# Kernel tuning notes

Hardware: AMD Instinct MI355X
Metric: run time of the kernel (lower is better)

## Reference

```python
import jax, jax.numpy as jnp
import numpy as np

WS = 7   # w_size
K = 9    # k_neighbors


def setup_inputs() -> dict:
    key = jax.random.key(0)
    ks = jax.random.split(key, 6)
    B, C, H, W = 16, 64, 112, 112
    Cf = C // 4
    return {
        'x_in': jax.random.normal(ks[0], (B, C, H, W), jnp.float32),
        'Wf': jax.random.normal(ks[1], (Cf, C), jnp.float32) / np.sqrt(C).astype(np.float32),
        'bf': jnp.zeros((Cf,), jnp.float32),
        'Wp': jax.random.normal(ks[2], (C, Cf), jnp.float32) / np.sqrt(Cf).astype(np.float32),
        'bp': jnp.zeros((C,), jnp.float32),
        'W1': jax.random.normal(ks[3], (4, 2), jnp.float32) / np.sqrt(2.0).astype(np.float32),
        'b1': jnp.zeros((4,), jnp.float32),
        'W2': jax.random.normal(ks[4], (1, 4), jnp.float32) / 2.0,
        'b2': jnp.zeros((1,), jnp.float32),
        'sigma': jnp.asarray(4.0, jnp.float32),
        'alpha': jnp.asarray(0.5, jnp.float32),
    }


def reference(x_in, Wf, bf, Wp, bp, W1, b1, W2, b2, sigma, alpha):
    B, C, H, W = x_in.shape
    w, h = H // WS, W // WS                      # per-window spatial dims
    Bp, N = B * WS * WS, w * h                   # num windows, nodes per window
    # window partition: b c (Wg w) (Hg h) -> (b Wg Hg) c w h
    x = x_in.reshape(B, C, WS, w, WS, h).transpose(0, 2, 4, 1, 3, 5).reshape(Bp, C, w, h)
    # 1x1 conv f: dim -> dim//4
    f = jnp.einsum('bchw,oc->bohw', x, Wf) + bf[None, :, None, None]
    Cf = f.shape[1]
    xf = f.reshape(Bp, Cf, N).transpose(0, 2, 1)          # [Bp, N, Cf] node features
    # all-pairs cosine similarity (torch eps=1e-8)
    xn = xf / jnp.maximum(jnp.linalg.norm(xf, axis=-1, keepdims=True), 1e-8)
    sim_feat = jnp.einsum('bnc,bmc->bnm', xn, xn)         # [Bp, N, N]
    # spatial gaussian similarity
    ii, jj = jnp.meshgrid(jnp.arange(w), jnp.arange(h), indexing='ij')
    coords = jnp.stack([ii, jj], -1).reshape(N, 2).astype(jnp.float32)
    dist = jnp.sqrt(jnp.sum((coords[:, None] - coords[None]) ** 2, -1))
    sim_dist = jnp.exp(-dist ** 2 / (2.0 * sigma ** 2))   # [N, N]
    combined = alpha * sim_feat + (1.0 - alpha) * sim_dist[None]
    _, idx = jax.lax.top_k(combined, K)                   # [Bp, N, K] neighbor ids
    # gather neighbor messages; edges of node n are exactly its K top-k columns
    msg = xf[jnp.arange(Bp)[:, None, None], idx]          # [Bp, N, K, Cf]
    sf = jnp.take_along_axis(sim_feat, idx, axis=-1)      # edge cosine sim
    sd = sim_dist[jnp.arange(N)[:, None], idx]            # edge spatial sim
    pair = jnp.stack([sf, sd], -1)                        # [Bp, N, K, 2]
    hdn = jax.nn.silu(pair @ W1.T + b1)
    wgt = jax.nn.sigmoid(hdn @ W2.T + b2)[..., 0]         # [Bp, N, K]
    # scatter_add over edge_index[0] == per-source sum over its K edges
    wn = wgt / (jnp.sum(wgt, -1, keepdims=True) + 1e-12)
    out = jnp.einsum('bnk,bnkc->bnc', wn, msg)            # [Bp, N, Cf]
    out = out.reshape(Bp, w, h, Cf).transpose(0, 3, 1, 2)
    # window un-partition: (b Wg Hg) c w h -> b c (Wg w) (Hg h)
    out = out.reshape(B, WS, WS, Cf, w, h).transpose(0, 3, 1, 4, 2, 5).reshape(B, Cf, H, W)
    # 1x1 conv p: dim//4 -> dim, then flatten(2)
    y = jnp.einsum('bchw,oc->bohw', out, Wp) + bp[None, :, None, None]
    return y.reshape(B, C, H * W)
```

## Files before the change

kernel.cpp:

```cpp
#include <hip/hip_runtime.h>
#include <math.h>

#define CC    64
#define CF    16
#define NPIX  256
#define KK    9
#define HWQ   12544
#define WWQ   112
#define NTILE 784
#define MBLK  128

__global__ __launch_bounds__(64, 4) void feat_k(
    const float* __restrict__ x_in, const float* __restrict__ Wf,
    const float* __restrict__ bf,
    float* __restrict__ xn_g, float* __restrict__ nrm_g)
{
    __shared__ float s_Wt[CC * CF];
    __shared__ float s_bf[CF];
    const int tid = threadIdx.x;
    for (int idx = tid; idx < CC * CF; idx += 64) {
        int c = idx >> 4, o = idx & 15;
        s_Wt[idx] = Wf[o * CC + c];
    }
    if (tid < CF) s_bf[tid] = bf[tid];
    __syncthreads();

    const int p    = blockIdx.x * 64 + tid;
    const int tile = p >> 8, pix = p & 255;
    const int bb = tile / 49, ssb = tile % 49;
    const int s1 = ssb / 7, s2 = ssb % 7;
    const int gy = s1 * 16 + (pix >> 4), gx = s2 * 16 + (pix & 15);
    const float* xb = x_in + (size_t)bb * CC * HWQ + (size_t)gy * WWQ + gx;

    float fv[CF];
    #pragma unroll
    for (int o = 0; o < CF; ++o) fv[o] = 0.0f;
    #pragma unroll 8
    for (int c = 0; c < CC; ++c) {
        float xv = xb[(size_t)c * HWQ];
        const float4* w4 = reinterpret_cast<const float4*>(&s_Wt[c << 4]);
        float4 w0 = w4[0], w1 = w4[1], w2 = w4[2], w3 = w4[3];
        fv[0]  = fmaf(xv, w0.x, fv[0]);  fv[1]  = fmaf(xv, w0.y, fv[1]);
        fv[2]  = fmaf(xv, w0.z, fv[2]);  fv[3]  = fmaf(xv, w0.w, fv[3]);
        fv[4]  = fmaf(xv, w1.x, fv[4]);  fv[5]  = fmaf(xv, w1.y, fv[5]);
        fv[6]  = fmaf(xv, w1.z, fv[6]);  fv[7]  = fmaf(xv, w1.w, fv[7]);
        fv[8]  = fmaf(xv, w2.x, fv[8]);  fv[9]  = fmaf(xv, w2.y, fv[9]);
        fv[10] = fmaf(xv, w2.z, fv[10]); fv[11] = fmaf(xv, w2.w, fv[11]);
        fv[12] = fmaf(xv, w3.x, fv[12]); fv[13] = fmaf(xv, w3.y, fv[13]);
        fv[14] = fmaf(xv, w3.z, fv[14]); fv[15] = fmaf(xv, w3.w, fv[15]);
    }
    #pragma unroll
    for (int o = 0; o < CF; ++o) fv[o] += s_bf[o];

    float ss2 = 0.0f;
    #pragma unroll
    for (int o = 0; o < CF; ++o) ss2 = fmaf(fv[o], fv[o], ss2);
    float nrm = fmaxf(sqrtf(ss2), 1e-8f);

    float xn[CF];
    #pragma unroll
    for (int o = 0; o < CF; ++o) xn[o] = fv[o] / nrm;

    float4* dst = reinterpret_cast<float4*>(xn_g + (size_t)p * CF);
    dst[0] = make_float4(xn[0],  xn[1],  xn[2],  xn[3]);
    dst[1] = make_float4(xn[4],  xn[5],  xn[6],  xn[7]);
    dst[2] = make_float4(xn[8],  xn[9],  xn[10], xn[11]);
    dst[3] = make_float4(xn[12], xn[13], xn[14], xn[15]);
    nrm_g[p] = nrm;
}

#define DOT16(dot, a0, a1, a2, a3)                                   \
    dot = fmaf(xnr[0],  (a0).x, dot); dot = fmaf(xnr[1],  (a0).y, dot); \
    dot = fmaf(xnr[2],  (a0).z, dot); dot = fmaf(xnr[3],  (a0).w, dot); \
    dot = fmaf(xnr[4],  (a1).x, dot); dot = fmaf(xnr[5],  (a1).y, dot); \
    dot = fmaf(xnr[6],  (a1).z, dot); dot = fmaf(xnr[7],  (a1).w, dot); \
    dot = fmaf(xnr[8],  (a2).x, dot); dot = fmaf(xnr[9],  (a2).y, dot); \
    dot = fmaf(xnr[10], (a2).z, dot); dot = fmaf(xnr[11], (a2).w, dot); \
    dot = fmaf(xnr[12], (a3).x, dot); dot = fmaf(xnr[13], (a3).y, dot); \
    dot = fmaf(xnr[14], (a3).z, dot); dot = fmaf(xnr[15], (a3).w, dot);

#define TOP9_INSERT(cv, ci) {                                        \
    const bool g0 = (cv) > tv0; const bool g1 = (cv) > tv1;          \
    const bool g2 = (cv) > tv2; const bool g3 = (cv) > tv3;          \
    const bool g4 = (cv) > tv4; const bool g5 = (cv) > tv5;          \
    const bool g6 = (cv) > tv6; const bool g7 = (cv) > tv7;          \
    const bool g8 = (cv) > tv8;                                      \
    const float nv0 = g0 ? (cv) : tv0;                               \
    const float nv1 = __builtin_amdgcn_fmed3f((cv), tv0, tv1);       \
    const float nv2 = __builtin_amdgcn_fmed3f((cv), tv1, tv2);       \
    const float nv3 = __builtin_amdgcn_fmed3f((cv), tv2, tv3);       \
    const float nv4 = __builtin_amdgcn_fmed3f((cv), tv3, tv4);       \
    const float nv5 = __builtin_amdgcn_fmed3f((cv), tv4, tv5);       \
    const float nv6 = __builtin_amdgcn_fmed3f((cv), tv5, tv6);       \
    const float nv7 = __builtin_amdgcn_fmed3f((cv), tv6, tv7);       \
    const float nv8 = __builtin_amdgcn_fmed3f((cv), tv7, tv8);       \
    const int nt0 = g0 ? (ci) : ti0;                                 \
    const int nt1 = g0 ? ti0 : (g1 ? (ci) : ti1);                    \
    const int nt2 = g1 ? ti1 : (g2 ? (ci) : ti2);                    \
    const int nt3 = g2 ? ti2 : (g3 ? (ci) : ti3);                    \
    const int nt4 = g3 ? ti3 : (g4 ? (ci) : ti4);                    \
    const int nt5 = g4 ? ti4 : (g5 ? (ci) : ti5);                    \
    const int nt6 = g5 ? ti5 : (g6 ? (ci) : ti6);                    \
    const int nt7 = g6 ? ti6 : (g7 ? (ci) : ti7);                    \
    const int nt8 = g7 ? ti7 : (g8 ? (ci) : ti8);                    \
    tv0 = nv0; tv1 = nv1; tv2 = nv2; tv3 = nv3; tv4 = nv4;           \
    tv5 = nv5; tv6 = nv6; tv7 = nv7; tv8 = nv8;                      \
    ti0 = nt0; ti1 = nt1; ti2 = nt2; ti3 = nt3; ti4 = nt4;           \
    ti5 = nt5; ti6 = nt6; ti7 = nt7; ti8 = nt8; }

#define SIM_ITER(MJ) {                                               \
    const int m = mbase + (MJ);                                      \
    const float4* xm4 = reinterpret_cast<const float4*>(&s_xn[m][0]);\
    const float4 a0 = xm4[0], a1 = xm4[1], a2 = xm4[2], a3 = xm4[3]; \
    float dot = 0.0f;                                                \
    DOT16(dot, a0, a1, a2, a3);                                      \
    const int dj = pj - (MJ);                                        \
    const float sdA = s_tabA[d2i + dj * dj];                         \
    const float comb = __fadd_rn(__fmul_rn(alpha, dot), sdA);        \
    TOP9_INSERT(comb, m); }

__global__ __launch_bounds__(MBLK, 4) void gnn_main(
    const float* __restrict__ xn_g, const float* __restrict__ nrm_g,
    const float* __restrict__ Wp,   const float* __restrict__ bp,
    const float* __restrict__ W1,   const float* __restrict__ b1,
    const float* __restrict__ W2,   const float* __restrict__ b2,
    const float* __restrict__ sigma_p, const float* __restrict__ alpha_p,
    float* __restrict__ y)
{
    __shared__ float s_xn[NPIX][CF];
    __shared__ float s_nrm[NPIX];
    __shared__ float s_tab[451];
    __shared__ float s_tabA[451];

    const int bid  = blockIdx.x;
    const int tile = bid >> 1;
    const int hlf  = bid & 1;
    const int bb = tile / 49, ssb = tile % 49;
    const int s1 = ssb / 7, s2 = ssb % 7;
    const int tid = threadIdx.x;

    const float alpha = alpha_p[0];
    const float oma   = 1.0f - alpha;
    const float sig   = sigma_p[0];
    const float denom = 2.0f * sig * sig;

    for (int t = tid; t < 451; t += MBLK) {
        float dd = sqrtf((float)t);
        float v  = expf((-(dd * dd)) / denom);
        s_tab[t]  = v;
        s_tabA[t] = __fmul_rn(oma, v);
    }
    const float* xt = xn_g + (size_t)tile * NPIX * CF;
    {
        const float4* src = reinterpret_cast<const float4*>(xt);
        float4*       dst = reinterpret_cast<float4*>(&s_xn[0][0]);
        #pragma unroll
        for (int i = 0; i < 8; ++i) dst[tid + i * MBLK] = src[tid + i * MBLK];
        const float* nsrc = nrm_g + (size_t)tile * NPIX;
        s_nrm[tid]        = nsrc[tid];
        s_nrm[tid + MBLK] = nsrc[tid + MBLK];
    }
    float W1r[8], b1r[4], W2r[4];
    #pragma unroll
    for (int h = 0; h < 8; ++h) W1r[h] = W1[h];
    #pragma unroll
    for (int h = 0; h < 4; ++h) { b1r[h] = b1[h]; W2r[h] = W2[h]; }
    const float b2r = b2[0];
    __syncthreads();

    const int r  = hlf * MBLK + tid;
    const int pi = r >> 4, pj = r & 15;

    float xnr[CF];
    {
        const float4* xr4 = reinterpret_cast<const float4*>(&s_xn[r][0]);
        float4 r0 = xr4[0], r1 = xr4[1], r2 = xr4[2], r3 = xr4[3];
        xnr[0]=r0.x;  xnr[1]=r0.y;  xnr[2]=r0.z;  xnr[3]=r0.w;
        xnr[4]=r1.x;  xnr[5]=r1.y;  xnr[6]=r1.z;  xnr[7]=r1.w;
        xnr[8]=r2.x;  xnr[9]=r2.y;  xnr[10]=r2.z; xnr[11]=r2.w;
        xnr[12]=r3.x; xnr[13]=r3.y; xnr[14]=r3.z; xnr[15]=r3.w;
    }

    float tv0,tv1,tv2,tv3,tv4,tv5,tv6,tv7,tv8;
    int   ti0,ti1,ti2,ti3,ti4,ti5,ti6,ti7,ti8;
    tv0=tv1=tv2=tv3=tv4=tv5=tv6=tv7=tv8 = -INFINITY;
    ti0=ti1=ti2=ti3=ti4=ti5=ti6=ti7=ti8 = 0;

    #pragma unroll 1
    for (int mi = 0; mi < 16; ++mi) {
        const int di  = pi - mi;
        const int d2i = di * di;
        const int mbase = mi << 4;
        SIM_ITER(0)  SIM_ITER(1)  SIM_ITER(2)  SIM_ITER(3)
        SIM_ITER(4)  SIM_ITER(5)  SIM_ITER(6)  SIM_ITER(7)
        SIM_ITER(8)  SIM_ITER(9)  SIM_ITER(10) SIM_ITER(11)
        SIM_ITER(12) SIM_ITER(13) SIM_ITER(14) SIM_ITER(15)
    }

    const float tv[KK] = {tv0,tv1,tv2,tv3,tv4,tv5,tv6,tv7,tv8};
    const int   ti[KK] = {ti0,ti1,ti2,ti3,ti4,ti5,ti6,ti7,ti8};

    float wk[KK];
    float wsum = 0.0f;
    #pragma unroll
    for (int k = 0; k < KK; ++k) {
        int m = ti[k];
        int di = pi - (m >> 4);
        int dj = pj - (m & 15);
        float sd = s_tab[di * di + dj * dj];
        float sf = (tv[k] - __fmul_rn(oma, sd)) / alpha;
        float hsum = b2r;
        #pragma unroll
        for (int h = 0; h < 4; ++h) {
            float z  = fmaf(sf, W1r[2 * h], fmaf(sd, W1r[2 * h + 1], b1r[h]));
            float sg = 1.0f / (1.0f + expf(-z));
            hsum = fmaf(z * sg, W2r[h], hsum);
        }
        float wg = 1.0f / (1.0f + expf(-hsum));
        wk[k] = wg;
        wsum += wg;
    }
    wsum += 1e-12f;

    float outv[CF];
    #pragma unroll
    for (int o = 0; o < CF; ++o) outv[o] = 0.0f;
    #pragma unroll
    for (int k = 0; k < KK; ++k) {
        const int m = ti[k];
        const float wnm = (wk[k] / wsum) * s_nrm[m];
        const float4* xf4 = reinterpret_cast<const float4*>(&s_xn[m][0]);
        float4 m0 = xf4[0], m1 = xf4[1], m2 = xf4[2], m3 = xf4[3];
        outv[0]  = fmaf(wnm, m0.x, outv[0]);  outv[1]  = fmaf(wnm, m0.y, outv[1]);
        outv[2]  = fmaf(wnm, m0.z, outv[2]);  outv[3]  = fmaf(wnm, m0.w, outv[3]);
        outv[4]  = fmaf(wnm, m1.x, outv[4]);  outv[5]  = fmaf(wnm, m1.y, outv[5]);
        outv[6]  = fmaf(wnm, m1.z, outv[6]);  outv[7]  = fmaf(wnm, m1.w, outv[7]);
        outv[8]  = fmaf(wnm, m2.x, outv[8]);  outv[9]  = fmaf(wnm, m2.y, outv[9]);
        outv[10] = fmaf(wnm, m2.z, outv[10]); outv[11] = fmaf(wnm, m2.w, outv[11]);
        outv[12] = fmaf(wnm, m3.x, outv[12]); outv[13] = fmaf(wnm, m3.y, outv[13]);
        outv[14] = fmaf(wnm, m3.z, outv[14]); outv[15] = fmaf(wnm, m3.w, outv[15]);
    }

    const int gy = s1 * 16 + pi, gx = s2 * 16 + pj;
    float* yb = y + (size_t)bb * CC * HWQ + (size_t)gy * WWQ + gx;
    #pragma unroll 4
    for (int o = 0; o < CC; ++o) {
        const float4* w4 = reinterpret_cast<const float4*>(&Wp[o * CF]);
        float4 w0 = w4[0], w1 = w4[1], w2 = w4[2], w3 = w4[3];
        float acc = 0.0f;
        acc = fmaf(outv[0],  w0.x, acc); acc = fmaf(outv[1],  w0.y, acc);
        acc = fmaf(outv[2],  w0.z, acc); acc = fmaf(outv[3],  w0.w, acc);
        acc = fmaf(outv[4],  w1.x, acc); acc = fmaf(outv[5],  w1.y, acc);
        acc = fmaf(outv[6],  w1.z, acc); acc = fmaf(outv[7],  w1.w, acc);
        acc = fmaf(outv[8],  w2.x, acc); acc = fmaf(outv[9],  w2.y, acc);
        acc = fmaf(outv[10], w2.z, acc); acc = fmaf(outv[11], w2.w, acc);
        acc = fmaf(outv[12], w3.x, acc); acc = fmaf(outv[13], w3.y, acc);
        acc = fmaf(outv[14], w3.z, acc); acc = fmaf(outv[15], w3.w, acc);
        yb[(size_t)o * HWQ] = acc + bp[o];
    }
}

__global__ __launch_bounds__(256) void gnn_fused(
    const float* __restrict__ x_in, const float* __restrict__ Wf,
    const float* __restrict__ bf,   const float* __restrict__ Wp,
    const float* __restrict__ bp,   const float* __restrict__ W1,
    const float* __restrict__ b1,   const float* __restrict__ W2,
    const float* __restrict__ b2,   const float* __restrict__ sigma_p,
    const float* __restrict__ alpha_p, float* __restrict__ y)
{
    __shared__ float s_xf[NPIX][CF];
    __shared__ float s_xn[NPIX][CF];
    __shared__ float s_W[CC * CF];
    __shared__ float s_table[451];
    __shared__ float s_bias[CC];

    const int bpi = blockIdx.x;
    const int bb  = bpi / 49;
    const int ssb = bpi % 49;
    const int s1  = ssb / 7, s2 = ssb % 7;
    const int tid = threadIdx.x;
    const int pi  = tid >> 4, pj = tid & 15;
    const int gy  = s1 * 16 + pi, gx = s2 * 16 + pj;

    const float alpha = alpha_p[0];
    const float oma   = 1.0f - alpha;
    const float sig   = sigma_p[0];
    const float denom = 2.0f * sig * sig;

    for (int t = tid; t < CF * CC; t += NPIX) s_W[t] = Wf[t];
    if (tid < CF) s_bias[tid] = bf[tid];
    for (int t = tid; t < 451; t += NPIX) {
        float dd = sqrtf((float)t);
        s_table[t] = expf((-(dd * dd)) / denom);
    }
    float W1r[8], b1r[4], W2r[4];
    #pragma unroll
    for (int h = 0; h < 8; ++h) W1r[h] = W1[h];
    #pragma unroll
    for (int h = 0; h < 4; ++h) { b1r[h] = b1[h]; W2r[h] = W2[h]; }
    const float b2r = b2[0];
    __syncthreads();

    const float* xb = x_in + (size_t)bb * CC * HWQ + (size_t)gy * WWQ + gx;
    float fv[CF];
    #pragma unroll
    for (int o = 0; o < CF; ++o) fv[o] = 0.0f;
    for (int c = 0; c < CC; ++c) {
        float xv = xb[(size_t)c * HWQ];
        #pragma unroll
        for (int o = 0; o < CF; ++o)
            fv[o] = fmaf(xv, s_W[o * CC + c], fv[o]);
    }
    #pragma unroll
    for (int o = 0; o < CF; ++o) fv[o] += s_bias[o];

    float ss2 = 0.0f;
    #pragma unroll
    for (int o = 0; o < CF; ++o) ss2 = fmaf(fv[o], fv[o], ss2);
    float nrm = fmaxf(sqrtf(ss2), 1e-8f);

    float xnr[CF];
    #pragma unroll
    for (int o = 0; o < CF; ++o) {
        xnr[o] = fv[o] / nrm;
        s_xf[tid][o] = fv[o];
        s_xn[tid][o] = xnr[o];
    }
    __syncthreads();

    float tv[KK]; int ti[KK];
    #pragma unroll
    for (int k = 0; k < KK; ++k) { tv[k] = -INFINITY; ti[k] = 0; }

    for (int m = 0; m < NPIX; ++m) {
        const float4* xm4 = reinterpret_cast<const float4*>(&s_xn[m][0]);
        float4 a0 = xm4[0], a1 = xm4[1], a2 = xm4[2], a3 = xm4[3];
        float dot = 0.0f;
        dot = fmaf(xnr[0],  a0.x, dot); dot = fmaf(xnr[1],  a0.y, dot);
        dot = fmaf(xnr[2],  a0.z, dot); dot = fmaf(xnr[3],  a0.w, dot);
        dot = fmaf(xnr[4],  a1.x, dot); dot = fmaf(xnr[5],  a1.y, dot);
        dot = fmaf(xnr[6],  a1.z, dot); dot = fmaf(xnr[7],  a1.w, dot);
        dot = fmaf(xnr[8],  a2.x, dot); dot = fmaf(xnr[9],  a2.y, dot);
        dot = fmaf(xnr[10], a2.z, dot); dot = fmaf(xnr[11], a2.w, dot);
        dot = fmaf(xnr[12], a3.x, dot); dot = fmaf(xnr[13], a3.y, dot);
        dot = fmaf(xnr[14], a3.z, dot); dot = fmaf(xnr[15], a3.w, dot);

        int di = pi - (m >> 4);
        int dj = pj - (m & 15);
        float sd = s_table[di * di + dj * dj];
        float comb = __fadd_rn(__fmul_rn(alpha, dot), __fmul_rn(oma, sd));

        if (comb > tv[KK - 1]) {
            float cv = comb; int ci = m;
            #pragma unroll
            for (int t = KK - 1; t >= 0; --t) {
                bool g = (cv > tv[t]);
                float ov = tv[t]; int oi = ti[t];
                if (g) {
                    if (t + 1 < KK) { tv[t + 1] = ov; ti[t + 1] = oi; }
                    tv[t] = cv; ti[t] = ci;
                }
            }
        }
    }

    float wk[KK];
    float wsum = 0.0f;
    #pragma unroll
    for (int k = 0; k < KK; ++k) {
        int m = ti[k];
        int di = pi - (m >> 4);
        int dj = pj - (m & 15);
        float sd = s_table[di * di + dj * dj];
        float sf = (tv[k] - __fmul_rn(oma, sd)) / alpha;
        float hsum = b2r;
        #pragma unroll
        for (int h = 0; h < 4; ++h) {
            float z  = fmaf(sf, W1r[2 * h], fmaf(sd, W1r[2 * h + 1], b1r[h]));
            float sg = 1.0f / (1.0f + expf(-z));
            hsum = fmaf(z * sg, W2r[h], hsum);
        }
        float wg = 1.0f / (1.0f + expf(-hsum));
        wk[k] = wg;
        wsum += wg;
    }
    wsum += 1e-12f;

    float outv[CF];
    #pragma unroll
    for (int o = 0; o < CF; ++o) outv[o] = 0.0f;
    #pragma unroll
    for (int k = 0; k < KK; ++k) {
        float wn = wk[k] / wsum;
        int m = ti[k];
        const float4* xf4 = reinterpret_cast<const float4*>(&s_xf[m][0]);
        float4 m0 = xf4[0], m1 = xf4[1], m2 = xf4[2], m3 = xf4[3];
        outv[0]  = fmaf(wn, m0.x, outv[0]);  outv[1]  = fmaf(wn, m0.y, outv[1]);
        outv[2]  = fmaf(wn, m0.z, outv[2]);  outv[3]  = fmaf(wn, m0.w, outv[3]);
        outv[4]  = fmaf(wn, m1.x, outv[4]);  outv[5]  = fmaf(wn, m1.y, outv[5]);
        outv[6]  = fmaf(wn, m1.z, outv[6]);  outv[7]  = fmaf(wn, m1.w, outv[7]);
        outv[8]  = fmaf(wn, m2.x, outv[8]);  outv[9]  = fmaf(wn, m2.y, outv[9]);
        outv[10] = fmaf(wn, m2.z, outv[10]); outv[11] = fmaf(wn, m2.w, outv[11]);
        outv[12] = fmaf(wn, m3.x, outv[12]); outv[13] = fmaf(wn, m3.y, outv[13]);
        outv[14] = fmaf(wn, m3.z, outv[14]); outv[15] = fmaf(wn, m3.w, outv[15]);
    }

    __syncthreads();
    for (int t = tid; t < CC * CF; t += NPIX) s_W[t] = Wp[t];
    if (tid < CC) s_bias[tid] = bp[tid];
    __syncthreads();

    float* yb = y + (size_t)bb * CC * HWQ + (size_t)gy * WWQ + gx;
    for (int o = 0; o < CC; ++o) {
        float acc = 0.0f;
        #pragma unroll
        for (int c = 0; c < CF; ++c)
            acc = fmaf(outv[c], s_W[o * CF + c], acc);
        yb[(size_t)o * HWQ] = acc + s_bias[o];
    }
}

extern "C" void kernel_launch(void* const* d_in, const int* in_sizes, int n_in,
                              void* d_out, int out_size, void* d_ws, size_t ws_size,
                              hipStream_t stream) {
    const float* x_in  = (const float*)d_in[0];
    const float* Wf    = (const float*)d_in[1];
    const float* bf    = (const float*)d_in[2];
    const float* Wp    = (const float*)d_in[3];
    const float* bp    = (const float*)d_in[4];
    const float* W1    = (const float*)d_in[5];
    const float* b1    = (const float*)d_in[6];
    const float* W2    = (const float*)d_in[7];
    const float* b2    = (const float*)d_in[8];
    const float* sigma = (const float*)d_in[9];
    const float* alpha = (const float*)d_in[10];
    float* y = (float*)d_out;

    const size_t need = (size_t)(NTILE * NPIX * CF + NTILE * NPIX) * sizeof(float);
    if (ws_size >= need) {
        float* xn_g  = (float*)d_ws;
        float* nrm_g = xn_g + (size_t)NTILE * NPIX * CF;
        feat_k<<<3136, 64, 0, stream>>>(x_in, Wf, bf, xn_g, nrm_g);
        gnn_main<<<NTILE * 2, MBLK, 0, stream>>>(xn_g, nrm_g, Wp, bp, W1, b1,
                                                 W2, b2, sigma, alpha, y);
    } else {
        gnn_fused<<<NTILE, NPIX, 0, stream>>>(x_in, Wf, bf, Wp, bp, W1, b1, W2,
                                              b2, sigma, alpha, y);
    }
}
```

Before: 131.1 us.

## Split top-k candidate scan across two thread halves with global partial merge

Each block grows to 256 threads, and the two 128-thread halves scan disjoint halves of the 256 candidate nodes, so every row keeps its own partial top-9. The upper half writes its partial list to a new workspace buffer. After a block barrier the lower half reads it back and merges it with TOP9_INSERT before computing edge weights and the output projection. The aim is more parallelism and latency hiding in the serial similarity and top-k scan. In exchange it needs more workspace, adds global-memory traffic and a barrier, and tighter launch bounds that could cause register spills; the old path is kept as a fallback when workspace is small.

```diff
diff --git a/kernel.cpp b/kernel.cpp
--- a/kernel.cpp
+++ b/kernel.cpp
@@ -8,6 +8,7 @@
 #define HWQ   12544
 #define WWQ   112
 #define NTILE 784
+#define NROWS (NTILE * NPIX)
 #define MBLK  128
 
 __global__ __launch_bounds__(64, 4) void feat_k(
@@ -119,12 +120,19 @@
     const float comb = __fadd_rn(__fmul_rn(alpha, dot), sdA);        \
     TOP9_INSERT(comb, m); }
 
-__global__ __launch_bounds__(MBLK, 4) void gnn_main(
+#define SIM_ROW16()                                                  \
+        SIM_ITER(0)  SIM_ITER(1)  SIM_ITER(2)  SIM_ITER(3)           \
+        SIM_ITER(4)  SIM_ITER(5)  SIM_ITER(6)  SIM_ITER(7)           \
+        SIM_ITER(8)  SIM_ITER(9)  SIM_ITER(10) SIM_ITER(11)          \
+        SIM_ITER(12) SIM_ITER(13) SIM_ITER(14) SIM_ITER(15)
+
+__global__ __launch_bounds__(256, 7) void gnn_split(
     const float* __restrict__ xn_g, const float* __restrict__ nrm_g,
     const float* __restrict__ Wp,   const float* __restrict__ bp,
     const float* __restrict__ W1,   const float* __restrict__ b1,
     const float* __restrict__ W2,   const float* __restrict__ b2,
     const float* __restrict__ sigma_p, const float* __restrict__ alpha_p,
+    float* __restrict__ pval, int* __restrict__ pidx,
     float* __restrict__ y)
 {
     __shared__ float s_xn[NPIX][CF];
@@ -138,13 +146,15 @@
     const int bb = tile / 49, ssb = tile % 49;
     const int s1 = ssb / 7, s2 = ssb % 7;
     const int tid = threadIdx.x;
+    const int rl  = tid & 127;
+    const int ch  = tid >> 7;
 
     const float alpha = alpha_p[0];
     const float oma   = 1.0f - alpha;
     const float sig   = sigma_p[0];
     const float denom = 2.0f * sig * sig;
 
-    for (int t = tid; t < 451; t += MBLK) {
+    for (int t = tid; t < 451; t += 256) {
         float dd = sqrtf((float)t);
         float v  = expf((-(dd * dd)) / denom);
         s_tab[t]  = v;
@@ -155,10 +165,8 @@
         const float4* src = reinterpret_cast<const float4*>(xt);
         float4*       dst = reinterpret_cast<float4*>(&s_xn[0][0]);
         #pragma unroll
-        for (int i = 0; i < 8; ++i) dst[tid + i * MBLK] = src[tid + i * MBLK];
-        const float* nsrc = nrm_g + (size_t)tile * NPIX;
-        s_nrm[tid]        = nsrc[tid];
-        s_nrm[tid + MBLK] = nsrc[tid + MBLK];
+        for (int i = 0; i < 4; ++i) dst[tid + i * 256] = src[tid + i * 256];
+        s_nrm[tid] = nrm_g[(size_t)tile * NPIX + tid];
     }
     float W1r[8], b1r[4], W2r[4];
     #pragma unroll
@@ -168,8 +176,9 @@
     const float b2r = b2[0];
     __syncthreads();
 
-    const int r  = hlf * MBLK + tid;
+    const int r  = hlf * 128 + rl;
     const int pi = r >> 4, pj = r & 15;
+    const int gRow = tile * NPIX + r;
 
     float xnr[CF];
     {
@@ -186,15 +195,35 @@
     tv0=tv1=tv2=tv3=tv4=tv5=tv6=tv7=tv8 = -INFINITY;
     ti0=ti1=ti2=ti3=ti4=ti5=ti6=ti7=ti8 = 0;
 
+    const int mi0 = ch << 3;
     #pragma unroll 1
-    for (int mi = 0; mi < 16; ++mi) {
+    for (int q = 0; q < 8; ++q) {
+        const int mi  = mi0 + q;
         const int di  = pi - mi;
         const int d2i = di * di;
         const int mbase = mi << 4;
-        SIM_ITER(0)  SIM_ITER(1)  SIM_ITER(2)  SIM_ITER(3)
-        SIM_ITER(4)  SIM_ITER(5)  SIM_ITER(6)  SIM_ITER(7)
-        SIM_ITER(8)  SIM_ITER(9)  SIM_ITER(10) SIM_ITER(11)
-        SIM_ITER(12) SIM_ITER(13) SIM_ITER(14) SIM_ITER(15)
+        SIM_ROW16()
+    }
+
+    if (ch == 1) {
+        pval[0 * NROWS + gRow] = tv0; pidx[0 * NROWS + gRow] = ti0;
+        pval[1 * NROWS + gRow] = tv1; pidx[1 * NROWS + gRow] = ti1;
+        pval[2 * NROWS + gRow] = tv2; pidx[2 * NROWS + gRow] = ti2;
+        pval[3 * NROWS + gRow] = tv3; pidx[3 * NROWS + gRow] = ti3;
+        pval[4 * NROWS + gRow] = tv4; pidx[4 * NROWS + gRow] = ti4;
+        pval[5 * NROWS + gRow] = tv5; pidx[5 * NROWS + gRow] = ti5;
+        pval[6 * NROWS + gRow] = tv6; pidx[6 * NROWS + gRow] = ti6;
+        pval[7 * NROWS + gRow] = tv7; pidx[7 * NROWS + gRow] = ti7;
+        pval[8 * NROWS + gRow] = tv8; pidx[8 * NROWS + gRow] = ti8;
+    }
+    __syncthreads();
+    if (ch == 1) return;
+
+    #pragma unroll
+    for (int k = 0; k < KK; ++k) {
+        const float bv = pval[k * NROWS + gRow];
+        const int   bi = pidx[k * NROWS + gRow];
+        TOP9_INSERT(bv, bi);
     }
 
     const float tv[KK] = {tv0,tv1,tv2,tv3,tv4,tv5,tv6,tv7,tv8};
@@ -260,6 +289,144 @@
     }
 }
 
+__global__ __launch_bounds__(MBLK, 4) void gnn_main_r5(
+    const float* __restrict__ xn_g, const float* __restrict__ nrm_g,
+    const float* __restrict__ Wp,   const float* __restrict__ bp,
+    const float* __restrict__ W1,   const float* __restrict__ b1,
+    const float* __restrict__ W2,   const float* __restrict__ b2,
+    const float* __restrict__ sigma_p, const float* __restrict__ alpha_p,
+    float* __restrict__ y)
+{
+    __shared__ float s_xn[NPIX][CF];
+    __shared__ float s_nrm[NPIX];
+    __shared__ float s_tab[451];
+    __shared__ float s_tabA[451];
+
+    const int bid  = blockIdx.x;
+    const int tile = bid >> 1;
+    const int hlf  = bid & 1;
+    const int bb = tile / 49, ssb = tile % 49;
+    const int s1 = ssb / 7, s2 = ssb % 7;
+    const int tid = threadIdx.x;
+
+    const float alpha = alpha_p[0];
+    const float oma   = 1.0f - alpha;
+    const float sig   = sigma_p[0];
+    const float denom = 2.0f * sig * sig;
+
+    for (int t = tid; t < 451; t += MBLK) {
+        float dd = sqrtf((float)t);
+        float v  = expf((-(dd * dd)) / denom);
+        s_tab[t]  = v;
+        s_tabA[t] = __fmul_rn(oma, v);
+    }
+    const float* xt = xn_g + (size_t)tile * NPIX * CF;
+    {
+        const float4* src = reinterpret_cast<const float4*>(xt);
+        float4*       dst = reinterpret_cast<float4*>(&s_xn[0][0]);
+        #pragma unroll
+        for (int i = 0; i < 8; ++i) dst[tid + i * MBLK] = src[tid + i * MBLK];
+        const float* nsrc = nrm_g + (size_t)tile * NPIX;
+        s_nrm[tid]        = nsrc[tid];
+        s_nrm[tid + MBLK] = nsrc[tid + MBLK];
+    }
+    float W1r[8], b1r[4], W2r[4];
+    #pragma unroll
+    for (int h = 0; h < 8; ++h) W1r[h] = W1[h];
+    #pragma unroll
+    for (int h = 0; h < 4; ++h) { b1r[h] = b1[h]; W2r[h] = W2[h]; }
+    const float b2r = b2[0];
+    __syncthreads();
+
+    const int r  = hlf * MBLK + tid;
+    const int pi = r >> 4, pj = r & 15;
+
+    float xnr[CF];
+    {
+        const float4* xr4 = reinterpret_cast<const float4*>(&s_xn[r][0]);
+        float4 r0 = xr4[0], r1 = xr4[1], r2 = xr4[2], r3 = xr4[3];
+        xnr[0]=r0.x;  xnr[1]=r0.y;  xnr[2]=r0.z;  xnr[3]=r0.w;
+        xnr[4]=r1.x;  xnr[5]=r1.y;  xnr[6]=r1.z;  xnr[7]=r1.w;
+        xnr[8]=r2.x;  xnr[9]=r2.y;  xnr[10]=r2.z; xnr[11]=r2.w;
+        xnr[12]=r3.x; xnr[13]=r3.y; xnr[14]=r3.z; xnr[15]=r3.w;
+    }
+
+    float tv0,tv1,tv2,tv3,tv4,tv5,tv6,tv7,tv8;
+    int   ti0,ti1,ti2,ti3,ti4,ti5,ti6,ti7,ti8;
+    tv0=tv1=tv2=tv3=tv4=tv5=tv6=tv7=tv8 = -INFINITY;
+    ti0=ti1=ti2=ti3=ti4=ti5=ti6=ti7=ti8 = 0;
+
+    #pragma unroll 1
+    for (int mi = 0; mi < 16; ++mi) {
+        const int di  = pi - mi;
+        const int d2i = di * di;
+        const int mbase = mi << 4;
+        SIM_ROW16()
+    }
+
+    const float tv[KK] = {tv0,tv1,tv2,tv3,tv4,tv5,tv6,tv7,tv8};
+    const int   ti[KK] = {ti0,ti1,ti2,ti3,ti4,ti5,ti6,ti7,ti8};
+
+    float wk[KK];
+    float wsum = 0.0f;
+    #pragma unroll
+    for (int k = 0; k < KK; ++k) {
+        int m = ti[k];
+        int di = pi - (m >> 4);
+        int dj = pj - (m & 15);
+        float sd = s_tab[di * di + dj * dj];
+        float sf = (tv[k] - __fmul_rn(oma, sd)) / alpha;
+        float hsum = b2r;
+        #pragma unroll
+        for (int h = 0; h < 4; ++h) {
+            float z  = fmaf(sf, W1r[2 * h], fmaf(sd, W1r[2 * h + 1], b1r[h]));
+            float sg = 1.0f / (1.0f + expf(-z));
+            hsum = fmaf(z * sg, W2r[h], hsum);
+        }
+        float wg = 1.0f / (1.0f + expf(-hsum));
+        wk[k] = wg;
+        wsum += wg;
+    }
+    wsum += 1e-12f;
+
+    float outv[CF];
+    #pragma unroll
+    for (int o = 0; o < CF; ++o) outv[o] = 0.0f;
+    #pragma unroll
+    for (int k = 0; k < KK; ++k) {
+        const int m = ti[k];
+        const float wnm = (wk[k] / wsum) * s_nrm[m];
+        const float4* xf4 = reinterpret_cast<const float4*>(&s_xn[m][0]);
+        float4 m0 = xf4[0], m1 = xf4[1], m2 = xf4[2], m3 = xf4[3];
+        outv[0]  = fmaf(wnm, m0.x, outv[0]);  outv[1]  = fmaf(wnm, m0.y, outv[1]);
+        outv[2]  = fmaf(wnm, m0.z, outv[2]);  outv[3]  = fmaf(wnm, m0.w, outv[3]);
+        outv[4]  = fmaf(wnm, m1.x, outv[4]);  outv[5]  = fmaf(wnm, m1.y, outv[5]);
+        outv[6]  = fmaf(wnm, m1.z, outv[6]);  outv[7]  = fmaf(wnm, m1.w, outv[7]);
+        outv[8]  = fmaf(wnm, m2.x, outv[8]);  outv[9]  = fmaf(wnm, m2.y, outv[9]);
+        outv[10] = fmaf(wnm, m2.z, outv[10]); outv[11] = fmaf(wnm, m2.w, outv[11]);
+        outv[12] = fmaf(wnm, m3.x, outv[12]); outv[13] = fmaf(wnm, m3.y, outv[13]);
+        outv[14] = fmaf(wnm, m3.z, outv[14]); outv[15] = fmaf(wnm, m3.w, outv[15]);
+    }
+
+    const int gy = s1 * 16 + pi, gx = s2 * 16 + pj;
+    float* yb = y + (size_t)bb * CC * HWQ + (size_t)gy * WWQ + gx;
+    #pragma unroll 4
+    for (int o = 0; o < CC; ++o) {
+        const float4* w4 = reinterpret_cast<const float4*>(&Wp[o * CF]);
+        float4 w0 = w4[0], w1 = w4[1], w2 = w4[2], w3 = w4[3];
+        float acc = 0.0f;
+        acc = fmaf(outv[0],  w0.x, acc); acc = fmaf(outv[1],  w0.y, acc);
+        acc = fmaf(outv[2],  w0.z, acc); acc = fmaf(outv[3],  w0.w, acc);
+        acc = fmaf(outv[4],  w1.x, acc); acc = fmaf(outv[5],  w1.y, acc);
+        acc = fmaf(outv[6],  w1.z, acc); acc = fmaf(outv[7],  w1.w, acc);
+        acc = fmaf(outv[8],  w2.x, acc); acc = fmaf(outv[9],  w2.y, acc);
+        acc = fmaf(outv[10], w2.z, acc); acc = fmaf(outv[11], w2.w, acc);
+        acc = fmaf(outv[12], w3.x, acc); acc = fmaf(outv[13], w3.y, acc);
+        acc = fmaf(outv[14], w3.z, acc); acc = fmaf(outv[15], w3.w, acc);
+        yb[(size_t)o * HWQ] = acc + bp[o];
+    }
+}
+
 __global__ __launch_bounds__(256) void gnn_fused(
     const float* __restrict__ x_in, const float* __restrict__ Wf,
     const float* __restrict__ bf,   const float* __restrict__ Wp,
@@ -436,13 +603,23 @@
     const float* alpha = (const float*)d_in[10];
     float* y = (float*)d_out;
 
-    const size_t need = (size_t)(NTILE * NPIX * CF + NTILE * NPIX) * sizeof(float);
-    if (ws_size >= need) {
+    const size_t need1 = (size_t)(NROWS * (CF + 1)) * sizeof(float);
+    const size_t need2 = need1 + (size_t)(2 * KK * NROWS) * sizeof(float);
+    if (ws_size >= need2) {
         float* xn_g  = (float*)d_ws;
-        float* nrm_g = xn_g + (size_t)NTILE * NPIX * CF;
+        float* nrm_g = xn_g + (size_t)NROWS * CF;
+        float* pval  = nrm_g + NROWS;
+        int*   pidx  = (int*)(pval + (size_t)KK * NROWS);
         feat_k<<<3136, 64, 0, stream>>>(x_in, Wf, bf, xn_g, nrm_g);
-        gnn_main<<<NTILE * 2, MBLK, 0, stream>>>(xn_g, nrm_g, Wp, bp, W1, b1,
-                                                 W2, b2, sigma, alpha, y);
+        gnn_split<<<NTILE * 2, 256, 0, stream>>>(xn_g, nrm_g, Wp, bp, W1, b1,
+                                                 W2, b2, sigma, alpha,
+                                                 pval, pidx, y);
+    } else if (ws_size >= need1) {
+        float* xn_g  = (float*)d_ws;
+        float* nrm_g = xn_g + (size_t)NROWS * CF;
+        feat_k<<<3136, 64, 0, stream>>>(x_in, Wf, bf, xn_g, nrm_g);
+        gnn_main_r5<<<NTILE * 2, MBLK, 0, stream>>>(xn_g, nrm_g, Wp, bp, W1, b1,
+                                                    W2, b2, sigma, alpha, y);
     } else {
         gnn_fused<<<NTILE, NPIX, 0, stream>>>(x_in, Wf, bf, Wp, bp, W1, b1, W2,
                                               b2, sigma, alpha, y);
```

New measurement: 175.2 us. +33.6%, slower.

## Split top-k candidate scan across two thread halves and merge via shared memory

Applied to the files above, without the earlier changes.

Each block now runs 256 threads instead of 128. Two threads share each query row, and each scans half of the 256 candidate columns while keeping its own top-9 list. The upper half writes its partial top-9 to shared memory, and the lower half merges those entries into its own list before the edge-weight and output stages. This doubles thread-level parallelism on the serial scan-and-insert loop, which was the latency-bound core. The cost is extra shared memory, a barrier, a merge step, and half the threads sitting idle for the epilogue.

```diff
diff --git a/kernel.cpp b/kernel.cpp
--- a/kernel.cpp
+++ b/kernel.cpp
@@ -8,7 +8,7 @@
 #define HWQ   12544
 #define WWQ   112
 #define NTILE 784
-#define MBLK  128
+#define NROWS (NTILE * NPIX)
 
 __global__ __launch_bounds__(64, 4) void feat_k(
     const float* __restrict__ x_in, const float* __restrict__ Wf,
@@ -119,7 +119,13 @@
     const float comb = __fadd_rn(__fmul_rn(alpha, dot), sdA);        \
     TOP9_INSERT(comb, m); }
 
-__global__ __launch_bounds__(MBLK, 4) void gnn_main(
+#define SIM_ROW16()                                                  \
+        SIM_ITER(0)  SIM_ITER(1)  SIM_ITER(2)  SIM_ITER(3)           \
+        SIM_ITER(4)  SIM_ITER(5)  SIM_ITER(6)  SIM_ITER(7)           \
+        SIM_ITER(8)  SIM_ITER(9)  SIM_ITER(10) SIM_ITER(11)          \
+        SIM_ITER(12) SIM_ITER(13) SIM_ITER(14) SIM_ITER(15)
+
+__global__ __launch_bounds__(256, 4) void gnn_split(
     const float* __restrict__ xn_g, const float* __restrict__ nrm_g,
     const float* __restrict__ Wp,   const float* __restrict__ bp,
     const float* __restrict__ W1,   const float* __restrict__ b1,
@@ -131,6 +137,8 @@
     __shared__ float s_nrm[NPIX];
     __shared__ float s_tab[451];
     __shared__ float s_tabA[451];
+    __shared__ float s_pv[KK][128];
+    __shared__ int   s_pi[KK][128];
 
     const int bid  = blockIdx.x;
     const int tile = bid >> 1;
@@ -138,13 +146,15 @@
     const int bb = tile / 49, ssb = tile % 49;
     const int s1 = ssb / 7, s2 = ssb % 7;
     const int tid = threadIdx.x;
+    const int rl  = tid & 127;
+    const int ch  = tid >> 7;
 
     const float alpha = alpha_p[0];
     const float oma   = 1.0f - alpha;
     const float sig   = sigma_p[0];
     const float denom = 2.0f * sig * sig;
 
-    for (int t = tid; t < 451; t += MBLK) {
+    for (int t = tid; t < 451; t += 256) {
         float dd = sqrtf((float)t);
         float v  = expf((-(dd * dd)) / denom);
         s_tab[t]  = v;
@@ -155,10 +165,8 @@
         const float4* src = reinterpret_cast<const float4*>(xt);
         float4*       dst = reinterpret_cast<float4*>(&s_xn[0][0]);
         #pragma unroll
-        for (int i = 0; i < 8; ++i) dst[tid + i * MBLK] = src[tid + i * MBLK];
-        const float* nsrc = nrm_g + (size_t)tile * NPIX;
-        s_nrm[tid]        = nsrc[tid];
-        s_nrm[tid + MBLK] = nsrc[tid + MBLK];
+        for (int i = 0; i < 4; ++i) dst[tid + i * 256] = src[tid + i * 256];
+        s_nrm[tid] = nrm_g[(size_t)tile * NPIX + tid];
     }
     float W1r[8], b1r[4], W2r[4];
     #pragma unroll
@@ -168,7 +176,7 @@
     const float b2r = b2[0];
     __syncthreads();
 
-    const int r  = hlf * MBLK + tid;
+    const int r  = hlf * 128 + rl;
     const int pi = r >> 4, pj = r & 15;
 
     float xnr[CF];
@@ -186,15 +194,35 @@
     tv0=tv1=tv2=tv3=tv4=tv5=tv6=tv7=tv8 = -INFINITY;
     ti0=ti1=ti2=ti3=ti4=ti5=ti6=ti7=ti8 = 0;
 
+    const int mi0 = ch << 3;
     #pragma unroll 1
-    for (int mi = 0; mi < 16; ++mi) {
+    for (int q = 0; q < 8; ++q) {
+        const int mi  = mi0 + q;
         const int di  = pi - mi;
         const int d2i = di * di;
         const int mbase = mi << 4;
-        SIM_ITER(0)  SIM_ITER(1)  SIM_ITER(2)  SIM_ITER(3)
-        SIM_ITER(4)  SIM_ITER(5)  SIM_ITER(6)  SIM_ITER(7)
-        SIM_ITER(8)  SIM_ITER(9)  SIM_ITER(10) SIM_ITER(11)
-        SIM_ITER(12) SIM_ITER(13) SIM_ITER(14) SIM_ITER(15)
+        SIM_ROW16()
+    }
+
+    if (ch == 1) {
+        s_pv[0][rl] = tv0; s_pi[0][rl] = ti0;
+        s_pv[1][rl] = tv1; s_pi[1][rl] = ti1;
+        s_pv[2][rl] = tv2; s_pi[2][rl] = ti2;
+        s_pv[3][rl] = tv3; s_pi[3][rl] = ti3;
+        s_pv[4][rl] = tv4; s_pi[4][rl] = ti4;
+        s_pv[5][rl] = tv5; s_pi[5][rl] = ti5;
+        s_pv[6][rl] = tv6; s_pi[6][rl] = ti6;
+        s_pv[7][rl] = tv7; s_pi[7][rl] = ti7;
+        s_pv[8][rl] = tv8; s_pi[8][rl] = ti8;
+    }
+    __syncthreads();
+    if (ch == 1) return;
+
+    #pragma unroll
+    for (int k = 0; k < KK; ++k) {
+        const float bv = s_pv[k][rl];
+        const int   bi = s_pi[k][rl];
+        TOP9_INSERT(bv, bi);
     }
 
     const float tv[KK] = {tv0,tv1,tv2,tv3,tv4,tv5,tv6,tv7,tv8};
@@ -436,12 +464,12 @@
     const float* alpha = (const float*)d_in[10];
     float* y = (float*)d_out;
 
-    const size_t need = (size_t)(NTILE * NPIX * CF + NTILE * NPIX) * sizeof(float);
+    const size_t need = (size_t)(NROWS * (CF + 1)) * sizeof(float);
     if (ws_size >= need) {
         float* xn_g  = (float*)d_ws;
-        float* nrm_g = xn_g + (size_t)NTILE * NPIX * CF;
+        float* nrm_g = xn_g + (size_t)NROWS * CF;
         feat_k<<<3136, 64, 0, stream>>>(x_in, Wf, bf, xn_g, nrm_g);
-        gnn_main<<<NTILE * 2, MBLK, 0, stream>>>(xn_g, nrm_g, Wp, bp, W1, b1,
+        gnn_split<<<NTILE * 2, 256, 0, stream>>>(xn_g, nrm_g, Wp, bp, W1, b1,
                                                  W2, b2, sigma, alpha, y);
     } else {
         gnn_fused<<<NTILE, NPIX, 0, stream>>>(x_in, Wf, bf, Wp, bp, W1, b1, W2,
```

New measurement: 129.4 us. No clear change (-1.4%).
